# Kernel optimization log

Measured on AMD Instinct MI355X. Metric: run time of the kernel, lower is better.

Reference implementation:

```python
import jax, jax.numpy as jnp
import numpy as np

N_NODES = 100000
N_EDGES = 1600000
NUM_GRAPHS = 4096
EPS = 1e-5


def _glorot(key, shape):
    fan_in, fan_out = shape[0], shape[1]
    lim = float(np.sqrt(6.0 / (fan_in + fan_out)))
    return jax.random.uniform(key, shape, jnp.float32, -lim, lim)


def setup_inputs() -> dict:
    key = jax.random.key(0)
    ks = jax.random.split(key, 32)
    inp = {}
    inp['x'] = jax.random.normal(ks[0], (N_NODES, 32), jnp.float32)
    inp['edge_attr'] = jax.random.uniform(ks[1], (N_EDGES, 8), jnp.float32)
    inp['edge_index'] = jax.random.randint(ks[2], (2, N_EDGES), 0, N_NODES, jnp.int32)
    inp['batch'] = jnp.sort(jax.random.randint(ks[3], (N_NODES,), 0, NUM_GRAPHS, jnp.int32))
    inp['num_graphs'] = NUM_GRAPHS
    # node/edge embeddings
    inp['Wn'] = _glorot(ks[4], (32, 64)); inp['bn_'] = jnp.zeros((64,), jnp.float32)
    inp['We'] = _glorot(ks[5], (8, 16)); inp['be_'] = jnp.zeros((16,), jnp.float32)
    # conv1: 2*64+16=144 -> 128 -> 64
    inp['W1a'] = _glorot(ks[6], (144, 128)); inp['b1a'] = jnp.zeros((128,), jnp.float32)
    inp['W1b'] = _glorot(ks[7], (128, 64)); inp['b1b'] = jnp.zeros((64,), jnp.float32)
    # conv2: 2*64+16=144 -> 64 -> 32
    inp['W2a'] = _glorot(ks[8], (144, 64)); inp['b2a'] = jnp.zeros((64,), jnp.float32)
    inp['W2b'] = _glorot(ks[9], (64, 32)); inp['b2b'] = jnp.zeros((32,), jnp.float32)
    # conv3: 2*32+16=80 -> 32 -> 16
    inp['W3a'] = _glorot(ks[10], (80, 32)); inp['b3a'] = jnp.zeros((32,), jnp.float32)
    inp['W3b'] = _glorot(ks[11], (32, 16)); inp['b3b'] = jnp.zeros((16,), jnp.float32)
    # batchnorm affine params
    inp['g1'] = jnp.ones((64,), jnp.float32); inp['beta1'] = jnp.zeros((64,), jnp.float32)
    inp['g2'] = jnp.ones((32,), jnp.float32); inp['beta2'] = jnp.zeros((32,), jnp.float32)
    inp['g3'] = jnp.ones((16,), jnp.float32); inp['beta3'] = jnp.zeros((16,), jnp.float32)
    # final fc 16 -> 12
    inp['Wfc'] = _glorot(ks[12], (16, 12)); inp['bfc'] = jnp.zeros((12,), jnp.float32)
    return inp


def _conv(x, e_emb, src, dst, Wa, ba, Wb, bb, n_nodes):
    # PyG: x_i = x[target]=x[dst], x_j = x[source]=x[src]; message MLP; mean-aggregate at dst
    m = jnp.concatenate([x[dst], x[src], e_emb], axis=1)      # [E, 2*in+edge]
    m = jax.nn.relu(m @ Wa + ba) @ Wb + bb                    # [E, out]
    s = jax.ops.segment_sum(m, dst, num_segments=n_nodes)
    cnt = jax.ops.segment_sum(jnp.ones((m.shape[0], 1), m.dtype), dst, num_segments=n_nodes)
    return s / jnp.maximum(cnt, 1.0)


def _batchnorm(x, g, b):
    mu = jnp.mean(x, axis=0)
    var = jnp.mean(jnp.square(x - mu), axis=0)
    return (x - mu) * jax.lax.rsqrt(var + EPS) * g + b


def reference(x, edge_attr, edge_index, batch, num_graphs,
              Wn, bn_, We, be_, W1a, b1a, W1b, b1b, W2a, b2a, W2b, b2b,
              W3a, b3a, W3b, b3b, g1, beta1, g2, beta2, g3, beta3, Wfc, bfc):
    n_nodes = x.shape[0]
    src, dst = edge_index[0], edge_index[1]
    e_emb = jax.nn.relu(edge_attr @ We + be_)                 # [E, 16]
    h = jax.nn.relu(x @ Wn + bn_)                             # [N, 64]
    h = _conv(h, e_emb, src, dst, W1a, b1a, W1b, b1b, n_nodes)
    h = jax.nn.relu(_batchnorm(h, g1, beta1))
    h = _conv(h, e_emb, src, dst, W2a, b2a, W2b, b2b, n_nodes)
    h = jax.nn.relu(_batchnorm(h, g2, beta2))
    h = _conv(h, e_emb, src, dst, W3a, b3a, W3b, b3b, n_nodes)
    h = jax.nn.relu(_batchnorm(h, g3, beta3))
    # global mean pool per graph
    s = jax.ops.segment_sum(h, batch, num_segments=num_graphs)
    cnt = jax.ops.segment_sum(jnp.ones((n_nodes, 1), h.dtype), batch, num_segments=num_graphs)
    pooled = s / jnp.maximum(cnt, 1.0)                        # [G, 16]
    return jax.nn.sigmoid(pooled @ Wfc + bfc)                 # [G, 12]
```

## Files before the change

### kernel.cpp

```cpp
#include <hip/hip_runtime.h>
#include <hip/hip_bf16.h>
#include <cstdio>


#define N_NODES 100000
#define N_EDGES 1600000
#define NUM_GRAPHS 4096

typedef unsigned short u16;
typedef unsigned int u32;
typedef _Float16 h2 __attribute__((ext_vector_type(2)));

#if defined(__has_builtin)
#if __has_builtin(__builtin_amdgcn_fdot2)
#define DOT2(a, b, c) __builtin_amdgcn_fdot2((a), (b), (c), false)
#endif
#endif
#ifndef DOT2
#define DOT2(a, b, c) ((c) + (float)(a).x * (float)(b).x + (float)(a).y * (float)(b).y)
#endif

__device__ __forceinline__ float b2f(u16 u) { union { u32 i; float f; } c; c.i = ((u32)u) << 16; return c.f; }
__device__ __forceinline__ float b2f_lo(u32 u) { union { u32 i; float f; } c; c.i = u << 16; return c.f; }
__device__ __forceinline__ float b2f_hi(u32 u) { union { u32 i; float f; } c; c.i = u & 0xffff0000u; return c.f; }
__device__ __forceinline__ u16 f2b(float f) {
    __hip_bfloat16 h = __float2bfloat16(f);
    return *reinterpret_cast<u16*>(&h);
}

template <int CPL>
__device__ __forceinline__ void ld_bf16(const u16* base, float out[CPL]) {
    if constexpr (CPL == 1) {
        out[0] = b2f(*base);
    } else {
        u32 v = *(const u32*)base;
        out[0] = b2f_lo(v); out[1] = b2f_hi(v);
    }
}
template <int CPL>
__device__ __forceinline__ void ld_f32(const float* base, float out[CPL]) {
    if constexpr (CPL == 1) {
        out[0] = *base;
    } else {
        float2 v = *(const float2*)base;
        out[0] = v.x; out[1] = v.y;
    }
}

__global__ __launch_bounds__(256) void hist_k(const int* __restrict__ dst, int* __restrict__ hist) {
    int e = blockIdx.x * 256 + threadIdx.x;
    if (e < N_EDGES) atomicAdd(&hist[dst[e]], 1);
}

__global__ __launch_bounds__(256) void scan_part_k(const int* __restrict__ hist,
        int* __restrict__ excl, int* __restrict__ bsum) {
    __shared__ int sm[256];
    int t = threadIdx.x, b = blockIdx.x;
    int base = b * 1024 + t * 4;
    int v0 = (base + 0 < N_NODES) ? hist[base + 0] : 0;
    int v1 = (base + 1 < N_NODES) ? hist[base + 1] : 0;
    int v2 = (base + 2 < N_NODES) ? hist[base + 2] : 0;
    int v3 = (base + 3 < N_NODES) ? hist[base + 3] : 0;
    int tsum = v0 + v1 + v2 + v3;
    sm[t] = tsum;
    __syncthreads();
    for (int o = 1; o < 256; o <<= 1) {
        int x = (t >= o) ? sm[t - o] : 0;
        __syncthreads();
        sm[t] += x;
        __syncthreads();
    }
    int texcl = sm[t] - tsum;
    if (base + 0 < N_NODES) excl[base + 0] = texcl;
    if (base + 1 < N_NODES) excl[base + 1] = texcl + v0;
    if (base + 2 < N_NODES) excl[base + 2] = texcl + v0 + v1;
    if (base + 3 < N_NODES) excl[base + 3] = texcl + v0 + v1 + v2;
    if (t == 255) bsum[b] = sm[255];
}

__global__ __launch_bounds__(256) void scan_top_k(int* __restrict__ bsum, int* __restrict__ boff,
        int nb, int* __restrict__ row_ptr_last) {
    __shared__ int sm[256];
    int t = threadIdx.x;
    int v = (t < nb) ? bsum[t] : 0;
    sm[t] = v;
    __syncthreads();
    for (int o = 1; o < 256; o <<= 1) {
        int x = (t >= o) ? sm[t - o] : 0;
        __syncthreads();
        sm[t] += x;
        __syncthreads();
    }
    if (t < nb) boff[t] = sm[t] - v;
    if (t == 0) *row_ptr_last = sm[255];
}

__global__ __launch_bounds__(256) void scan_add_k(int* __restrict__ excl, const int* __restrict__ boff,
        int* __restrict__ row_ptr, int* __restrict__ cursor) {
    int i = blockIdx.x * 256 + threadIdx.x;
    if (i >= N_NODES) return;
    int s = excl[i] + boff[i >> 10];
    row_ptr[i] = s;
    cursor[i] = s;
}

__global__ __launch_bounds__(256) void scatter_k(const int* __restrict__ src, const int* __restrict__ dst,
        int* __restrict__ cursor, int* __restrict__ sorted_eid, int* __restrict__ srcs) {
    int e = blockIdx.x * 256 + threadIdx.x;
    if (e < N_EDGES) {
        int p = atomicAdd(&cursor[dst[e]], 1);
        sorted_eid[p] = e;
        srcs[p] = src[e];
    }
}

__global__ __launch_bounds__(256) void edge_emb_k(const float* __restrict__ ea,
        const float* __restrict__ We, const float* __restrict__ be,
        const int* __restrict__ sorted_eid, _Float16* __restrict__ e16s) {
    int idx = blockIdx.x * 256 + threadIdx.x;
    if (idx >= N_EDGES * 16) return;
    int p = idx >> 4, k = idx & 15;
    int e = sorted_eid[p];
    float acc = be[k];
#pragma unroll
    for (int j = 0; j < 8; ++j) acc += ea[(size_t)e * 8 + j] * We[j * 16 + k];
    e16s[idx] = (_Float16)fmaxf(acc, 0.f);
}

__global__ __launch_bounds__(256) void node_emb_k(const float* __restrict__ x,
        const float* __restrict__ Wn, const float* __restrict__ bn_, float* __restrict__ h) {
    int idx = blockIdx.x * 256 + threadIdx.x;
    if (idx >= N_NODES * 64) return;
    int v = idx >> 6, c = idx & 63;
    float acc = bn_[c];
    for (int k = 0; k < 32; ++k) acc += x[(size_t)v * 32 + k] * Wn[(size_t)k * 64 + c];
    h[idx] = fmaxf(acc, 0.f);
}

template <int F, int H>
__global__ __launch_bounds__(256) void proj_k(const float* __restrict__ h,
        const float* __restrict__ Wa, const float* __restrict__ ba,
        float* __restrict__ Pd, u16* __restrict__ Ps) {
    constexpr int C2 = 2 * H;
    constexpr int NPB = 256 / C2;
    constexpr int TILE = 16 * NPB;
    __shared__ float hs[TILE][F];
    const int t = threadIdx.x;
    const int grp = t / C2;
    const int c = t % C2;
    const bool is_src = (c >= H);
    const int cc = is_src ? (c - H) : c;
    float w[F];
    const float* wcol = Wa + (size_t)(is_src ? F : 0) * H + cc;
#pragma unroll
    for (int k = 0; k < F; ++k) w[k] = wcol[(size_t)k * H];
    const float bias = is_src ? 0.f : ba[cc];

    for (int v0 = blockIdx.x * TILE; v0 < N_NODES; v0 += gridDim.x * TILE) {
        __syncthreads();
        for (int i = t; i < TILE * F; i += 256) {
            int vv = v0 + i / F;
            hs[i / F][i % F] = (vv < N_NODES) ? h[(size_t)vv * F + (i % F)] : 0.f;
        }
        __syncthreads();
        const int base = grp * 16;
        const int nmax = (N_NODES - v0 - base >= 16) ? 16
                        : (N_NODES - v0 - base > 0 ? N_NODES - v0 - base : 0);
#pragma unroll 2
        for (int n = 0; n < nmax; ++n) {
            const int v = v0 + base + n;
            const float4* hr4 = (const float4*)hs[base + n];
            float a0 = bias, a1 = 0.f, a2 = 0.f, a3 = 0.f;
#pragma unroll
            for (int k4 = 0; k4 < F / 4; ++k4) {
                float4 hv = hr4[k4];
                a0 += hv.x * w[4 * k4 + 0];
                a1 += hv.y * w[4 * k4 + 1];
                a2 += hv.z * w[4 * k4 + 2];
                a3 += hv.w * w[4 * k4 + 3];
            }
            float acc = (a0 + a1) + (a2 + a3);
            if (is_src) Ps[(size_t)v * H + cc] = f2b(acc);
            else        Pd[(size_t)v * H + cc] = acc;
        }
    }
}

template <int H>
__global__ __launch_bounds__(256) void conv_k(
        const int* __restrict__ row_ptr, const int* __restrict__ srcs,
        const _Float16* __restrict__ e16s,
        float* __restrict__ Pd, const u16* __restrict__ Ps,
        const float* __restrict__ Wae) {
    constexpr int SL = (H >= 64) ? 64 : 32;
    constexpr int NPW = 64 / SL;
    constexpr int CPL = H / SL;
    constexpr int NPB = 4 * NPW;
    const int wave = threadIdx.x >> 6, lane = threadIdx.x & 63;
    const int sub = lane / SL;
    const int sl = lane % SL;
    const int c0 = sl * CPL;
    h2 w2h[8][CPL];
#pragma unroll
    for (int k2 = 0; k2 < 8; ++k2)
#pragma unroll
        for (int j = 0; j < CPL; ++j) {
            h2 t;
            t.x = (_Float16)Wae[(2 * k2) * H + c0 + j];
            t.y = (_Float16)Wae[(2 * k2 + 1) * H + c0 + j];
            w2h[k2][j] = t;
        }

    for (int v = blockIdx.x * NPB + wave * NPW + sub; v < N_NODES; v += gridDim.x * NPB) {
        const int vv = (SL == 64) ? __builtin_amdgcn_readfirstlane(v) : v;
        float pd[CPL], acc[CPL];
        ld_f32<CPL>(&Pd[(size_t)vv * H + c0], pd);
#pragma unroll
        for (int j = 0; j < CPL; ++j) acc[j] = 0.f;
        const int p0 = row_ptr[vv], p1 = row_ptr[vv + 1];
        const int deg = p1 - p0;

        auto edge = [&](uint4 ra, uint4 rb, const float ps[CPL]) {
            union { u32 u; h2 h; } cv;
            h2 ev[8];
            cv.u = ra.x; ev[0] = cv.h; cv.u = ra.y; ev[1] = cv.h;
            cv.u = ra.z; ev[2] = cv.h; cv.u = ra.w; ev[3] = cv.h;
            cv.u = rb.x; ev[4] = cv.h; cv.u = rb.y; ev[5] = cv.h;
            cv.u = rb.z; ev[6] = cv.h; cv.u = rb.w; ev[7] = cv.h;
            float z[CPL];
#pragma unroll
            for (int j = 0; j < CPL; ++j) z[j] = pd[j] + ps[j];
#pragma unroll
            for (int k2 = 0; k2 < 8; ++k2)
#pragma unroll
                for (int j = 0; j < CPL; ++j) z[j] = DOT2(ev[k2], w2h[k2][j], z[j]);
#pragma unroll
            for (int j = 0; j < CPL; ++j) acc[j] += fmaxf(z[j], 0.f);
        };

        int p = p0;
        for (; p + 3 < p1; p += 4) {
            int s0 = srcs[p], s1 = srcs[p + 1], s2 = srcs[p + 2], s3 = srcs[p + 3];
            const uint4* e0 = (const uint4*)(e16s + (size_t)p * 16);
            uint4 a0 = e0[0], a1 = e0[1];
            uint4 b0 = e0[2], b1 = e0[3];
            uint4 g0 = e0[4], g1 = e0[5];
            uint4 d0 = e0[6], d1 = e0[7];
            float ps0[CPL], ps1[CPL], ps2[CPL], ps3[CPL];
            ld_bf16<CPL>(&Ps[(size_t)s0 * H + c0], ps0);
            ld_bf16<CPL>(&Ps[(size_t)s1 * H + c0], ps1);
            ld_bf16<CPL>(&Ps[(size_t)s2 * H + c0], ps2);
            ld_bf16<CPL>(&Ps[(size_t)s3 * H + c0], ps3);
            edge(a0, a1, ps0);
            edge(b0, b1, ps1);
            edge(g0, g1, ps2);
            edge(d0, d1, ps3);
        }
        for (; p < p1; ++p) {
            int s0 = srcs[p];
            const uint4* e0 = (const uint4*)(e16s + (size_t)p * 16);
            uint4 a0 = e0[0], a1 = e0[1];
            float ps0[CPL];
            ld_bf16<CPL>(&Ps[(size_t)s0 * H + c0], ps0);
            edge(a0, a1, ps0);
        }

        const float invd = (deg > 0) ? 1.f / (float)deg : 0.f;
        if constexpr (CPL == 2) {
            float2 o; o.x = acc[0] * invd; o.y = acc[1] * invd;
            *(float2*)&Pd[(size_t)vv * H + c0] = o;
        } else {
            Pd[(size_t)vv * H + c0] = acc[0] * invd;
        }
    }
}

template <int H, int Fo>
__global__ __launch_bounds__(256) void matvec_k(const float* __restrict__ m,
        const int* __restrict__ row_ptr,
        const float* __restrict__ Wb, const float* __restrict__ bb,
        float* __restrict__ y, float* __restrict__ stats) {
    constexpr int NPW = 64 / Fo;
    constexpr int NPB = 4 * NPW;
    __shared__ float sh[2 * Fo];
    if (threadIdx.x < 2 * Fo) sh[threadIdx.x] = 0.f;
    const int wave = threadIdx.x >> 6, lane = threadIdx.x & 63;
    const int sub = lane / Fo;
    const int c = lane % Fo;
    float w[H];
#pragma unroll
    for (int k = 0; k < H; ++k) w[k] = Wb[(size_t)k * Fo + c];
    const float bias = bb[c];
    float s1 = 0.f, s2 = 0.f;

    for (int v = blockIdx.x * NPB + wave * NPW + sub; v < N_NODES; v += gridDim.x * NPB) {
        const int deg = row_ptr[v + 1] - row_ptr[v];
        const float4* mr4 = (const float4*)(m + (size_t)v * H);
        float a0 = bias, a1 = 0.f, a2 = 0.f, a3 = 0.f;
#pragma unroll
        for (int k4 = 0; k4 < H / 4; ++k4) {
            float4 mv = mr4[k4];
            a0 += mv.x * w[4 * k4 + 0];
            a1 += mv.y * w[4 * k4 + 1];
            a2 += mv.z * w[4 * k4 + 2];
            a3 += mv.w * w[4 * k4 + 3];
        }
        float val = (deg > 0) ? (a0 + a1) + (a2 + a3) : 0.f;
        y[(size_t)v * Fo + c] = val;
        s1 += val; s2 += val * val;
    }
    __syncthreads();
    atomicAdd(&sh[c], s1);
    atomicAdd(&sh[Fo + c], s2);
    __syncthreads();
    if (threadIdx.x < 2 * Fo) atomicAdd(&stats[threadIdx.x], sh[threadIdx.x]);
}

template <int Fo>
__global__ __launch_bounds__(256) void bnrelu_k(float* __restrict__ y,
        const float* __restrict__ stats, const float* __restrict__ g, const float* __restrict__ beta) {
    int idx = blockIdx.x * 256 + threadIdx.x;
    if (idx >= N_NODES * Fo) return;
    int co = idx % Fo;
    const float invN = 1.0f / (float)N_NODES;
    float mu = stats[co] * invN;
    float ex2 = stats[Fo + co] * invN;
    float var = fmaxf(ex2 - mu * mu, 0.f);
    float rs = rsqrtf(var + 1e-5f);
    y[idx] = fmaxf((y[idx] - mu) * rs * g[co] + beta[co], 0.f);
}

__global__ __launch_bounds__(256) void pool_k(const float* __restrict__ h,
        const int* __restrict__ batch, float* __restrict__ pool, int* __restrict__ gcnt) {
    int idx = blockIdx.x * 256 + threadIdx.x;
    if (idx >= N_NODES * 16) return;
    int v = idx >> 4, c = idx & 15;
    int b = batch[v];
    atomicAdd(&pool[b * 16 + c], h[idx]);
    if (c == 0) atomicAdd(&gcnt[b], 1);
}

__global__ __launch_bounds__(256) void out_k(const float* __restrict__ pool,
        const int* __restrict__ gcnt, const float* __restrict__ Wfc,
        const float* __restrict__ bfc, float* __restrict__ out) {
    int idx = blockIdx.x * 256 + threadIdx.x;
    if (idx >= NUM_GRAPHS * 12) return;
    int g = idx / 12, o = idx % 12;
    int cnt = gcnt[g];
    float inv = 1.0f / (float)(cnt > 0 ? cnt : 1);
    float acc = bfc[o];
#pragma unroll
    for (int k = 0; k < 16; ++k) acc += pool[g * 16 + k] * inv * Wfc[k * 12 + o];
    out[idx] = 1.0f / (1.0f + expf(-acc));
}

extern "C" void kernel_launch(void* const* d_in, const int* in_sizes, int n_in,
                              void* d_out, int out_size, void* d_ws, size_t ws_size,
                              hipStream_t stream) {
    const size_t N = N_NODES, E = N_EDGES, G = NUM_GRAPHS;
    const float* x = (const float*)d_in[0];
    const float* ea = (const float*)d_in[1];
    const int* ei = (const int*)d_in[2];
    const int* srcv = ei;
    const int* dstv = ei + E;
    const int* batch = (const int*)d_in[3];
    const float* Wn = (const float*)d_in[5];  const float* bn_ = (const float*)d_in[6];
    const float* We = (const float*)d_in[7];  const float* be_ = (const float*)d_in[8];
    const float* W1a = (const float*)d_in[9]; const float* b1a = (const float*)d_in[10];
    const float* W1b = (const float*)d_in[11]; const float* b1b = (const float*)d_in[12];
    const float* W2a = (const float*)d_in[13]; const float* b2a = (const float*)d_in[14];
    const float* W2b = (const float*)d_in[15]; const float* b2b = (const float*)d_in[16];
    const float* W3a = (const float*)d_in[17]; const float* b3a = (const float*)d_in[18];
    const float* W3b = (const float*)d_in[19]; const float* b3b = (const float*)d_in[20];
    const float* g1 = (const float*)d_in[21]; const float* be1 = (const float*)d_in[22];
    const float* g2 = (const float*)d_in[23]; const float* be2 = (const float*)d_in[24];
    const float* g3 = (const float*)d_in[25]; const float* be3 = (const float*)d_in[26];
    const float* Wfc = (const float*)d_in[27]; const float* bfc = (const float*)d_in[28];

    char* base = (char*)d_ws;
    size_t off = 0;
    auto take = [&](size_t bytes) { size_t o = off; off += (bytes + 255) & ~(size_t)255; return o; };
    int* hist = (int*)(base + take(N * 4));
    int* cursor = (int*)(base + take(N * 4));
    int* row_ptr = (int*)(base + take((N + 1) * 4));
    int* bsum = (int*)(base + take(256 * 4));
    int* boff = (int*)(base + take(256 * 4));
    int* sorted = (int*)(base + take(E * 4));
    int* srcs = (int*)(base + take(E * 4));
    float* hbuf = (float*)(base + take(N * 64 * 4));
    float* Pd = (float*)(base + take(N * 128 * 4));
    u16* Ps = (u16*)(base + take(N * 128 * 2));
    _Float16* e16s = (_Float16*)(base + take(E * 16 * 2));
    float* stats = (float*)(base + take(256 * 4));
    float* pool = (float*)(base + take(G * 16 * 4));
    int* gcnt = (int*)(base + take(G * 4));
    if (off > ws_size) {
        fprintf(stderr, "kernel_launch: ws too small: need %zu have %zu\n", off, ws_size);
        return;
    }

    const int NB = (N_NODES + 1023) / 1024;

    hipMemsetAsync(hist, 0, N * 4, stream);
    hist_k<<<dim3((E + 255) / 256), dim3(256), 0, stream>>>(dstv, hist);
    scan_part_k<<<dim3(NB), dim3(256), 0, stream>>>(hist, cursor, bsum);
    scan_top_k<<<dim3(1), dim3(256), 0, stream>>>(bsum, boff, NB, &row_ptr[N_NODES]);
    scan_add_k<<<dim3((N + 255) / 256), dim3(256), 0, stream>>>(cursor, boff, row_ptr, cursor);
    scatter_k<<<dim3((E + 255) / 256), dim3(256), 0, stream>>>(srcv, dstv, cursor, sorted, srcs);

    edge_emb_k<<<dim3((E * 16 + 255) / 256), dim3(256), 0, stream>>>(ea, We, be_, sorted, e16s);
    node_emb_k<<<dim3((N * 64 + 255) / 256), dim3(256), 0, stream>>>(x, Wn, bn_, hbuf);

    proj_k<64, 128><<<dim3(6250), dim3(256), 0, stream>>>(hbuf, W1a, b1a, Pd, Ps);
    conv_k<128><<<dim3(3072), dim3(256), 0, stream>>>(row_ptr, srcs, e16s, Pd, Ps, W1a + 128 * 128);
    hipMemsetAsync(stats, 0, 256 * 4, stream);
    matvec_k<128, 64><<<dim3(1024), dim3(256), 0, stream>>>(Pd, row_ptr, W1b, b1b, hbuf, stats);
    bnrelu_k<64><<<dim3((N * 64 + 255) / 256), dim3(256), 0, stream>>>(hbuf, stats, g1, be1);

    proj_k<64, 64><<<dim3(3125), dim3(256), 0, stream>>>(hbuf, W2a, b2a, Pd, Ps);
    conv_k<64><<<dim3(3072), dim3(256), 0, stream>>>(row_ptr, srcs, e16s, Pd, Ps, W2a + 128 * 64);
    hipMemsetAsync(stats, 0, 256 * 4, stream);
    matvec_k<64, 32><<<dim3(1024), dim3(256), 0, stream>>>(Pd, row_ptr, W2b, b2b, hbuf, stats);
    bnrelu_k<32><<<dim3((N * 32 + 255) / 256), dim3(256), 0, stream>>>(hbuf, stats, g2, be2);

    proj_k<32, 32><<<dim3(1563), dim3(256), 0, stream>>>(hbuf, W3a, b3a, Pd, Ps);
    conv_k<32><<<dim3(3072), dim3(256), 0, stream>>>(row_ptr, srcs, e16s, Pd, Ps, W3a + 64 * 32);
    hipMemsetAsync(stats, 0, 256 * 4, stream);
    matvec_k<32, 16><<<dim3(1024), dim3(256), 0, stream>>>(Pd, row_ptr, W3b, b3b, hbuf, stats);
    bnrelu_k<16><<<dim3((N * 16 + 255) / 256), dim3(256), 0, stream>>>(hbuf, stats, g3, be3);

    hipMemsetAsync(pool, 0, G * 16 * 4, stream);
    hipMemsetAsync(gcnt, 0, G * 4, stream);
    pool_k<<<dim3((N * 16 + 255) / 256), dim3(256), 0, stream>>>(hbuf, batch, pool, gcnt);
    out_k<<<dim3((G * 12 + 255) / 256), dim3(256), 0, stream>>>(pool, gcnt, Wfc, bfc, (float*)d_out);
}
```

Measured before the change: 1.105 ms.

## Stage node tiles in LDS and split K across half-waves in matvec

The per-node output matvec no longer has each thread read whole rows of m straight from global memory with strided per-thread float4 loads. Blocks now cooperatively load a contiguous tile of 4096 floats (plus row_ptr entries) into shared memory with coalesced loads. The K dimension is split between the two half-waves, which are combined with a shuffle, halving each thread's weight registers. This improves global-load coalescing and register pressure, at the cost of extra LDS traffic, barriers and shuffles.

```diff
diff --git a/kernel.cpp b/kernel.cpp
--- a/kernel.cpp
+++ b/kernel.cpp
@@ -276,44 +276,92 @@
 }
 
 template <int H, int Fo>
-__global__ __launch_bounds__(256) void matvec_k(const float* __restrict__ m,
+__global__ __launch_bounds__(256) void matvec2_k(const float* __restrict__ m,
         const int* __restrict__ row_ptr,
         const float* __restrict__ Wb, const float* __restrict__ bb,
         float* __restrict__ y, float* __restrict__ stats) {
-    constexpr int NPW = 64 / Fo;
-    constexpr int NPB = 4 * NPW;
+    constexpr int FoC = (Fo < 32) ? Fo : 32;
+    constexpr int CG = Fo / FoC;
+    constexpr int NPW = 32 / FoC;
+    constexpr int NG = 4 / CG;
+    constexpr int SLOTS = NG * NPW;
+    constexpr int KH = H / 2;
+    constexpr int TILE = 4096 / H;
+    constexpr int J = TILE / SLOTS;
+
+    __shared__ float hs[TILE * H];
+    __shared__ int ptile[TILE + 1];
     __shared__ float sh[2 * Fo];
-    if (threadIdx.x < 2 * Fo) sh[threadIdx.x] = 0.f;
-    const int wave = threadIdx.x >> 6, lane = threadIdx.x & 63;
-    const int sub = lane / Fo;
-    const int c = lane % Fo;
-    float w[H];
-#pragma unroll
-    for (int k = 0; k < H; ++k) w[k] = Wb[(size_t)k * Fo + c];
+
+    const int t = threadIdx.x;
+    const int wave = t >> 6, lane = t & 63;
+    const int kh = lane >> 5;
+    const int r = lane & 31;
+    const int c_lo = r % FoC;
+    const int s = r / FoC;
+    const int cg = wave % CG;
+    const int ng = wave / CG;
+    const int c = cg * FoC + c_lo;
+    const int slot = ng * NPW + s;
+
+    for (int i = t; i < 2 * Fo; i += 256) sh[i] = 0.f;
+
+    float w[KH];
+#pragma unroll
+    for (int k = 0; k < KH; ++k) w[k] = Wb[(size_t)(kh * KH + k) * Fo + c];
     const float bias = bb[c];
     float s1 = 0.f, s2 = 0.f;
 
-    for (int v = blockIdx.x * NPB + wave * NPW + sub; v < N_NODES; v += gridDim.x * NPB) {
-        const int deg = row_ptr[v + 1] - row_ptr[v];
-        const float4* mr4 = (const float4*)(m + (size_t)v * H);
-        float a0 = bias, a1 = 0.f, a2 = 0.f, a3 = 0.f;
-#pragma unroll
-        for (int k4 = 0; k4 < H / 4; ++k4) {
-            float4 mv = mr4[k4];
-            a0 += mv.x * w[4 * k4 + 0];
-            a1 += mv.y * w[4 * k4 + 1];
-            a2 += mv.z * w[4 * k4 + 2];
-            a3 += mv.w * w[4 * k4 + 3];
-        }
-        float val = (deg > 0) ? (a0 + a1) + (a2 + a3) : 0.f;
-        y[(size_t)v * Fo + c] = val;
-        s1 += val; s2 += val * val;
-    }
+    const float4* msrc = (const float4*)m;
+    float4* hs4 = (float4*)hs;
+
+    for (int v0 = blockIdx.x * TILE; v0 < N_NODES; v0 += gridDim.x * TILE) {
+        __syncthreads();
+#pragma unroll
+        for (int q = t; q < 1024; q += 256) {
+            int node = (q * 4) / H;
+            float4 val;
+            if (v0 + node < N_NODES) val = msrc[(size_t)v0 * (H / 4) + q];
+            else { val.x = val.y = val.z = val.w = 0.f; }
+            hs4[q] = val;
+        }
+        for (int i = t; i <= TILE; i += 256) {
+            int v = v0 + i;
+            ptile[i] = row_ptr[v < N_NODES ? v : N_NODES];
+        }
+        __syncthreads();
+
+        for (int j = 0; j < J; ++j) {
+            const int n = slot + j * SLOTS;
+            const int v = v0 + n;
+            const float4* hr4 = (const float4*)&hs[n * H + kh * KH];
+            float a0 = 0.f, a1 = 0.f, a2 = 0.f, a3 = 0.f;
+#pragma unroll
+            for (int k4 = 0; k4 < KH / 4; ++k4) {
+                float4 hv = hr4[k4];
+                a0 += hv.x * w[4 * k4 + 0];
+                a1 += hv.y * w[4 * k4 + 1];
+                a2 += hv.z * w[4 * k4 + 2];
+                a3 += hv.w * w[4 * k4 + 3];
+            }
+            float half = (a0 + a1) + (a2 + a3);
+            float total = half + __shfl_xor(half, 32) + bias;
+            if (kh == 0 && v < N_NODES) {
+                const int deg = ptile[n + 1] - ptile[n];
+                float val = (deg > 0) ? total : 0.f;
+                y[(size_t)v * Fo + c] = val;
+                s1 += val; s2 += val * val;
+            }
+        }
+    }
+
     __syncthreads();
-    atomicAdd(&sh[c], s1);
-    atomicAdd(&sh[Fo + c], s2);
+    if (kh == 0) {
+        atomicAdd(&sh[c], s1);
+        atomicAdd(&sh[Fo + c], s2);
+    }
     __syncthreads();
-    if (threadIdx.x < 2 * Fo) atomicAdd(&stats[threadIdx.x], sh[threadIdx.x]);
+    if (t < 2 * Fo) atomicAdd(&stats[t], sh[t]);
 }
 
 template <int Fo>
@@ -414,19 +462,19 @@
     proj_k<64, 128><<<dim3(6250), dim3(256), 0, stream>>>(hbuf, W1a, b1a, Pd, Ps);
     conv_k<128><<<dim3(3072), dim3(256), 0, stream>>>(row_ptr, srcs, e16s, Pd, Ps, W1a + 128 * 128);
     hipMemsetAsync(stats, 0, 256 * 4, stream);
-    matvec_k<128, 64><<<dim3(1024), dim3(256), 0, stream>>>(Pd, row_ptr, W1b, b1b, hbuf, stats);
+    matvec2_k<128, 64><<<dim3(1024), dim3(256), 0, stream>>>(Pd, row_ptr, W1b, b1b, hbuf, stats);
     bnrelu_k<64><<<dim3((N * 64 + 255) / 256), dim3(256), 0, stream>>>(hbuf, stats, g1, be1);
 
     proj_k<64, 64><<<dim3(3125), dim3(256), 0, stream>>>(hbuf, W2a, b2a, Pd, Ps);
     conv_k<64><<<dim3(3072), dim3(256), 0, stream>>>(row_ptr, srcs, e16s, Pd, Ps, W2a + 128 * 64);
     hipMemsetAsync(stats, 0, 256 * 4, stream);
-    matvec_k<64, 32><<<dim3(1024), dim3(256), 0, stream>>>(Pd, row_ptr, W2b, b2b, hbuf, stats);
+    matvec2_k<64, 32><<<dim3(1024), dim3(256), 0, stream>>>(Pd, row_ptr, W2b, b2b, hbuf, stats);
     bnrelu_k<32><<<dim3((N * 32 + 255) / 256), dim3(256), 0, stream>>>(hbuf, stats, g2, be2);
 
     proj_k<32, 32><<<dim3(1563), dim3(256), 0, stream>>>(hbuf, W3a, b3a, Pd, Ps);
     conv_k<32><<<dim3(3072), dim3(256), 0, stream>>>(row_ptr, srcs, e16s, Pd, Ps, W3a + 64 * 32);
     hipMemsetAsync(stats, 0, 256 * 4, stream);
-    matvec_k<32, 16><<<dim3(1024), dim3(256), 0, stream>>>(Pd, row_ptr, W3b, b3b, hbuf, stats);
+    matvec2_k<32, 16><<<dim3(1024), dim3(256), 0, stream>>>(Pd, row_ptr, W3b, b3b, hbuf, stats);
     bnrelu_k<16><<<dim3((N * 16 + 255) / 256), dim3(256), 0, stream>>>(hbuf, stats, g3, be3);
 
     hipMemsetAsync(pool, 0, G * 16 * 4, stream);
```

After: 1.023 ms. -7.4%, faster.
